# Kernel optimization log

Hardware: AMD Instinct MI355X
Metric: run time of the kernel (lower is better)

## Reference

```python
import jax, jax.numpy as jnp
import numpy as np
import math

IN_F = 1024
OUT_F = 1024
B = 16
L = 4096  # img_size (number of positions)


def setup_inputs() -> dict:
    key = jax.random.key(0)
    k1, k2, k3 = jax.random.split(key, 3)
    Efou = jax.random.normal(k1, (B, L, IN_F), dtype=jnp.float32)
    y = jax.random.normal(k2, (B, IN_F), dtype=jnp.float32)
    weight = jax.random.normal(k3, (1, OUT_F, IN_F, 1), dtype=jnp.float32)
    return {"Efou": Efou, "y": y, "weight": weight}


def reference(Efou, y, weight):
    b, img_size, in_f = Efou.shape
    out_f = weight.shape[1]
    scale = 1.0 / math.sqrt(in_f)
    # per-sample modulated weights: [B, out, in]
    w = scale * weight[:, :, :, 0] * y[:, None, :]
    # demodulation norm over the input-feature axis
    dnorm = jax.lax.rsqrt(jnp.sum(w * w, axis=2, keepdims=True) + 1e-8)  # [B, out, 1]
    w = w * dnorm
    # faithful to torch: Efou.reshape(1, B*in, L) is a raw row-major reshape
    E = Efou.reshape(b, in_f, img_size)  # [B, in, L] (same bytes as original)
    x = jnp.einsum('boi,bil->bol', w, E)  # grouped conv1d, kernel size 1
    # faithful to torch: x.view(B, L, out) is a raw reshape of [B, out, L]
    return x.reshape(b, img_size, out_f)
```

## Files before the change

kernel.cpp:

```cpp
#include <hip/hip_runtime.h>
#include <hip/hip_bf16.h>
#include <cstdint>
#include <cstddef>

typedef __bf16 bf16x8 __attribute__((ext_vector_type(8)));
typedef __bf16 bf16x4 __attribute__((ext_vector_type(4)));
typedef float f32x4 __attribute__((ext_vector_type(4)));

#define BATCH 16
#define MDIM 1024
#define NDIM 4096
#define KDIM 1024
#define BM 256
#define BN 256
#define BK 64
#define NKT (KDIM / BK)

__device__ __forceinline__ void gload_lds16(const void* g, void* l) {
  __builtin_amdgcn_global_load_lds(
      (const __attribute__((address_space(1))) void*)g,
      (__attribute__((address_space(3))) void*)l, 16, 0, 0);
}

#define BAR() __builtin_amdgcn_s_barrier()
#define SB() __builtin_amdgcn_sched_barrier(0)
#define FENCE() asm volatile("" ::: "memory")
#define LGKM0()                                        \
  do {                                                 \
    asm volatile("s_waitcnt lgkmcnt(0)" ::: "memory"); \
    SB();                                              \
  } while (0)
#define VMC32()                                        \
  do {                                                 \
    asm volatile("s_waitcnt vmcnt(32)" ::: "memory");  \
    SB();                                              \
  } while (0)
#define VMC0()                                         \
  do {                                                 \
    asm volatile("s_waitcnt vmcnt(0)" ::: "memory");   \
    SB();                                              \
  } while (0)

__global__ __launch_bounds__(256) void modw_kernel(
    const float* __restrict__ weight, const float* __restrict__ y,
    __bf16* __restrict__ wm) {
  const int blk = blockIdx.x;
  const int b = blk & 15;
  const int o = blk >> 4;
  const int t = threadIdx.x;
  const float4 w4 = reinterpret_cast<const float4*>(weight + (size_t)o * KDIM)[t];
  const float4 y4 = reinterpret_cast<const float4*>(y + (size_t)b * KDIM)[t];
  const float p0 = w4.x * y4.x, p1 = w4.y * y4.y;
  const float p2 = w4.z * y4.z, p3 = w4.w * y4.w;
  float s = p0 * p0 + p1 * p1 + p2 * p2 + p3 * p3;
#pragma unroll
  for (int off = 32; off >= 1; off >>= 1) s += __shfl_xor(s, off, 64);
  __shared__ float ps[4];
  if ((t & 63) == 0) ps[t >> 6] = s;
  __syncthreads();
  const float tot = ps[0] + ps[1] + ps[2] + ps[3];
  const float scale = 0.03125f;
  const float dn = scale * rsqrtf(scale * scale * tot + 1e-8f);
  bf16x4 v;
  v[0] = (__bf16)(p0 * dn);
  v[1] = (__bf16)(p1 * dn);
  v[2] = (__bf16)(p2 * dn);
  v[3] = (__bf16)(p3 * dn);
  *reinterpret_cast<bf16x4*>(wm + ((size_t)b * MDIM + o) * KDIM + t * 4) = v;
}

__global__ __launch_bounds__(512, 2) void gemm_kernel(
    const __bf16* __restrict__ Wm, const float* __restrict__ E,
    float* __restrict__ out) {
  const int orig = blockIdx.x;
  const int wg = (orig & 7) * 128 + (orig >> 3);
  const int mt = wg & 3;
  const int nt = (wg >> 2) & 15;
  const int b = wg >> 6;
  const int m0 = mt * BM, n0 = nt * BN;

  __shared__ __align__(16) char smem[131072];
  char* const A0_ = smem;
  char* const A1_ = smem + 32768;
  char* const B0_ = smem + 65536;
  char* const B1_ = smem + 98304;

  const int tid = threadIdx.x;
  const int lane = tid & 63;
  const int wid = tid >> 6;
  const int wr = wid >> 2;
  const int wc = wid & 3;
  const int ml = lane & 15;
  const int kg = lane >> 4;

  const int arow = tid >> 3;
  const int aswz = ((tid & 7) ^ (arow & 7)) * 8;
  const __bf16* Ag = Wm + ((size_t)(b * MDIM + m0 + arow)) * KDIM + aswz;
  const int aldsOff = tid * 16;

  const int bn1 = tid & 63;
  const int bkg = tid >> 6;
  typedef const __attribute__((address_space(1))) float gfloat;
  gfloat* Eg = (gfloat*)(E + (size_t)b * KDIM * NDIM +
                         (size_t)(bkg * 8) * NDIM + n0 + bn1);
  int bwr[4];
#pragma unroll
  for (int c = 0; c < 4; ++c) {
    const int n = bn1 + 64 * c;
    bwr[c] = n * 128 + ((bkg * 16) ^ ((n & 7) << 4));
  }

  const int colA = (kg * 16) ^ ((ml & 7) << 4);
  const int arB = (wr * 128 + ml) * 128;
  const int brB = (wc * 64 + ml) * 128;

  f32x4 acc[8][4];
#pragma unroll
  for (int i = 0; i < 8; ++i)
#pragma unroll
    for (int j = 0; j < 4; ++j) acc[i][j] = (f32x4){0.f, 0.f, 0.f, 0.f};

  auto stageA = [&](char* Ab, int kt) {
#pragma unroll
    for (int r = 0; r < 4; ++r)
      gload_lds16(Ag + (size_t)(64 * r) * KDIM + kt * BK,
                  Ab + aldsOff + r * 8192);
  };
  auto loadB = [&](float (&brr)[4][8], int kt) {
#pragma unroll
    for (int c = 0; c < 4; ++c)
#pragma unroll
      for (int j = 0; j < 8; ++j)
        brr[c][j] = Eg[(size_t)(kt * BK + j) * NDIM + 64 * c];
  };
  auto writeB = [&](char* Bb, float (&brr)[4][8]) {
#pragma unroll
    for (int c = 0; c < 4; ++c) {
      bf16x8 v;
#pragma unroll
      for (int j = 0; j < 8; ++j) v[j] = (__bf16)brr[c][j];
      *reinterpret_cast<bf16x8*>(Bb + bwr[c]) = v;
    }
  };
  auto rdA = [&](bf16x8 (&d)[4], const char* Ab, int qm, int kk) {
#pragma unroll
    for (int i = 0; i < 4; ++i)
      d[i] = *reinterpret_cast<const bf16x8*>(Ab + arB + (qm * 4 + i) * 2048 +
                                              (colA ^ (kk * 64)));
  };
  auto rdB = [&](bf16x8 (&d)[4], const char* Bb, int kk) {
#pragma unroll
    for (int nf = 0; nf < 4; ++nf)
      d[nf] = *reinterpret_cast<const bf16x8*>(Bb + brB + nf * 2048 +
                                               (colA ^ (kk * 64)));
  };
  auto mfma16 = [&](bf16x8 (&a)[4], bf16x8 (&bv)[4], int qm) {
    __builtin_amdgcn_s_setprio(1);
#pragma unroll
    for (int i = 0; i < 4; ++i)
#pragma unroll
      for (int nf = 0; nf < 4; ++nf)
        acc[qm * 4 + i][nf] = __builtin_amdgcn_mfma_f32_16x16x32_bf16(
            a[i], bv[nf], acc[qm * 4 + i][nf], 0, 0, 0);
    __builtin_amdgcn_s_setprio(0);
  };

  float br[4][8];
  bf16x8 af0[4], af1[4];
  bf16x8 bf0[4], bf1[4];

  {
    float brT[4][8];
    stageA(A0_, 0);
    FENCE();
    loadB(brT, 0);
    writeB(B0_, brT);
    loadB(br, 1);
    LGKM0();
    BAR();
    rdA(af0, A0_, 0, 0);
    rdB(bf0, B0_, 0);
  }

  char* Ac = A0_;
  char* Ao = A1_;
  char* Bc = B0_;
  char* Bo = B1_;

#pragma unroll 1
  for (int t = 0; t < NKT; ++t) {
    const bool pf1 = (t + 1 < NKT);
    const bool pf2 = (t + 2 < NKT);

    rdA(af1, Ac, 1, 0);
    if (pf1) writeB(Bo, br);
    mfma16(af0, bf0, 0);

    rdB(bf1, Bc, 1);
    rdA(af0, Ac, 0, 1);
    if (pf1) stageA(Ao, t + 1);
    FENCE();
    if (pf2) loadB(br, t + 2);
    mfma16(af1, bf0, 1);

    rdA(af1, Ac, 1, 1);
    mfma16(af0, bf1, 0);
    LGKM0();
    if (pf2) {
      VMC32();
    } else {
      VMC0();
    }
    BAR();

    if (pf1) {
      rdA(af0, Ao, 0, 0);
      rdB(bf0, Bo, 0);
    }
    mfma16(af1, bf1, 1);

    char* ta = Ac; Ac = Ao; Ao = ta;
    char* tb = Bc; Bc = Bo; Bo = tb;
  }

  float* ob = out + ((size_t)(b * MDIM + m0 + wr * 128 + kg * 4)) * NDIM +
              n0 + wc * 64 + ml;
#pragma unroll
  for (int mf = 0; mf < 8; ++mf)
#pragma unroll
    for (int nf = 0; nf < 4; ++nf) {
      const f32x4 a = acc[mf][nf];
      float* p = ob + (size_t)mf * 16 * NDIM + nf * 16;
#pragma unroll
      for (int q = 0; q < 4; ++q) p[(size_t)q * NDIM] = a[q];
    }
}

extern "C" void kernel_launch(void* const* d_in, const int* in_sizes, int n_in,
                              void* d_out, int out_size, void* d_ws,
                              size_t ws_size, hipStream_t stream) {
  (void)in_sizes;
  (void)n_in;
  (void)out_size;
  (void)ws_size;
  const float* Efou = (const float*)d_in[0];
  const float* y = (const float*)d_in[1];
  const float* weight = (const float*)d_in[2];
  float* outp = (float*)d_out;
  __bf16* wm = (__bf16*)d_ws;

  modw_kernel<<<dim3(BATCH * MDIM), dim3(256), 0, stream>>>(weight, y, wm);
  gemm_kernel<<<dim3(BATCH * (MDIM / BM) * (NDIM / BN)), dim3(512), 0,
                stream>>>(wm, Efou, outp);
}
```

Measured before the change: 211.6 us.

## Triple-buffer the A tile in LDS with prefetch distance two, drop tail branches

Adds a third LDS buffer for the bf16 weight tile so A is staged two K-steps ahead, matching the register prefetch depth of the fp32 E loads. The tail-iteration branches are removed by wrapping the prefetch index, so every iteration issues the same 36 global loads and can use a fixed vmcnt(36) wait. This is meant to give A loads more time in flight and to keep the loop body uniform. In exchange, the last two iterations fetch data that is never used, and LDS use grows to 160KB per block.

```diff
diff --git a/kernel.cpp b/kernel.cpp
--- a/kernel.cpp
+++ b/kernel.cpp
@@ -30,14 +30,9 @@
     asm volatile("s_waitcnt lgkmcnt(0)" ::: "memory"); \
     SB();                                              \
   } while (0)
-#define VMC32()                                        \
+#define VMC36()                                        \
   do {                                                 \
-    asm volatile("s_waitcnt vmcnt(32)" ::: "memory");  \
-    SB();                                              \
-  } while (0)
-#define VMC0()                                         \
-  do {                                                 \
-    asm volatile("s_waitcnt vmcnt(0)" ::: "memory");   \
+    asm volatile("s_waitcnt vmcnt(36)" ::: "memory");  \
     SB();                                              \
   } while (0)
 
@@ -79,11 +74,12 @@
   const int b = wg >> 6;
   const int m0 = mt * BM, n0 = nt * BN;
 
-  __shared__ __align__(16) char smem[131072];
+  __shared__ __align__(16) char smem[163840];
   char* const A0_ = smem;
   char* const A1_ = smem + 32768;
-  char* const B0_ = smem + 65536;
-  char* const B1_ = smem + 98304;
+  char* const A2_ = smem + 65536;
+  char* const B0_ = smem + 98304;
+  char* const B1_ = smem + 131072;
 
   const int tid = threadIdx.x;
   const int lane = tid & 63;
@@ -176,50 +172,46 @@
     loadB(brT, 0);
     writeB(B0_, brT);
     loadB(br, 1);
+    FENCE();
+    stageA(A1_, 1);
     LGKM0();
     BAR();
     rdA(af0, A0_, 0, 0);
     rdB(bf0, B0_, 0);
   }
 
-  char* Ac = A0_;
-  char* Ao = A1_;
+  char* Acur = A0_;
+  char* Anxt = A1_;
+  char* Astg = A2_;
   char* Bc = B0_;
   char* Bo = B1_;
 
 #pragma unroll 1
   for (int t = 0; t < NKT; ++t) {
-    const bool pf1 = (t + 1 < NKT);
-    const bool pf2 = (t + 2 < NKT);
-
-    rdA(af1, Ac, 1, 0);
-    if (pf1) writeB(Bo, br);
+    const int t2 = (t + 2 < NKT) ? t + 2 : (t + 2 - NKT);
+
+    rdA(af1, Acur, 1, 0);
+    writeB(Bo, br);
     mfma16(af0, bf0, 0);
 
+    loadB(br, t2);
+    FENCE();
     rdB(bf1, Bc, 1);
-    rdA(af0, Ac, 0, 1);
-    if (pf1) stageA(Ao, t + 1);
-    FENCE();
-    if (pf2) loadB(br, t + 2);
+    rdA(af0, Acur, 0, 1);
+    stageA(Astg, t2);
     mfma16(af1, bf0, 1);
 
-    rdA(af1, Ac, 1, 1);
+    rdA(af1, Acur, 1, 1);
     mfma16(af0, bf1, 0);
     LGKM0();
-    if (pf2) {
-      VMC32();
-    } else {
-      VMC0();
-    }
+    VMC36();
     BAR();
 
-    if (pf1) {
-      rdA(af0, Ao, 0, 0);
-      rdB(bf0, Bo, 0);
-    }
+    rdA(af0, Anxt, 0, 0);
+    rdB(bf0, Bo, 0);
     mfma16(af1, bf1, 1);
 
-    char* ta = Ac; Ac = Ao; Ao = ta;
+    char* ta = Acur; Acur = Anxt; Anxt = Astg; Astg = ta;
     char* tb = Bc; Bc = Bo; Bo = tb;
   }
 
```

Result: no change. 212.5 us (+0.4%).

## Load A operand fragments directly from global memory instead of staging through LDS

Applied to the files above, without the earlier changes.

Removes the LDS double-buffer for the modulated-weight A tile and has each wave load its MFMA A fragments straight from global memory into registers. LDS use is halved and the explicit vmcnt waits and async global-to-LDS copies are dropped. In exchange, A data is no longer shared across the four column waves, so each block makes redundant global/L2 reads of A. Global-load latency now sits directly in the MFMA dependency chain, with only compiler-inserted waits to cover it.

```diff
diff --git a/kernel.cpp b/kernel.cpp
--- a/kernel.cpp
+++ b/kernel.cpp
@@ -16,28 +16,11 @@
 #define BK 64
 #define NKT (KDIM / BK)
 
-__device__ __forceinline__ void gload_lds16(const void* g, void* l) {
-  __builtin_amdgcn_global_load_lds(
-      (const __attribute__((address_space(1))) void*)g,
-      (__attribute__((address_space(3))) void*)l, 16, 0, 0);
-}
-
 #define BAR() __builtin_amdgcn_s_barrier()
 #define SB() __builtin_amdgcn_sched_barrier(0)
-#define FENCE() asm volatile("" ::: "memory")
 #define LGKM0()                                        \
   do {                                                 \
     asm volatile("s_waitcnt lgkmcnt(0)" ::: "memory"); \
-    SB();                                              \
-  } while (0)
-#define VMC32()                                        \
-  do {                                                 \
-    asm volatile("s_waitcnt vmcnt(32)" ::: "memory");  \
-    SB();                                              \
-  } while (0)
-#define VMC0()                                         \
-  do {                                                 \
-    asm volatile("s_waitcnt vmcnt(0)" ::: "memory");   \
     SB();                                              \
   } while (0)
 
@@ -79,11 +62,9 @@
   const int b = wg >> 6;
   const int m0 = mt * BM, n0 = nt * BN;
 
-  __shared__ __align__(16) char smem[131072];
-  char* const A0_ = smem;
-  char* const A1_ = smem + 32768;
-  char* const B0_ = smem + 65536;
-  char* const B1_ = smem + 98304;
+  __shared__ __align__(16) char smem[65536];
+  char* const B0_ = smem;
+  char* const B1_ = smem + 32768;
 
   const int tid = threadIdx.x;
   const int lane = tid & 63;
@@ -93,10 +74,8 @@
   const int ml = lane & 15;
   const int kg = lane >> 4;
 
-  const int arow = tid >> 3;
-  const int aswz = ((tid & 7) ^ (arow & 7)) * 8;
-  const __bf16* Ag = Wm + ((size_t)(b * MDIM + m0 + arow)) * KDIM + aswz;
-  const int aldsOff = tid * 16;
+  const __bf16* AgW =
+      Wm + ((size_t)(b * MDIM + m0 + wr * 128 + ml)) * KDIM + kg * 8;
 
   const int bn1 = tid & 63;
   const int bkg = tid >> 6;
@@ -111,7 +90,6 @@
   }
 
   const int colA = (kg * 16) ^ ((ml & 7) << 4);
-  const int arB = (wr * 128 + ml) * 128;
   const int brB = (wc * 64 + ml) * 128;
 
   f32x4 acc[8][4];
@@ -120,12 +98,6 @@
 #pragma unroll
     for (int j = 0; j < 4; ++j) acc[i][j] = (f32x4){0.f, 0.f, 0.f, 0.f};
 
-  auto stageA = [&](char* Ab, int kt) {
-#pragma unroll
-    for (int r = 0; r < 4; ++r)
-      gload_lds16(Ag + (size_t)(64 * r) * KDIM + kt * BK,
-                  Ab + aldsOff + r * 8192);
-  };
   auto loadB = [&](float (&brr)[4][8], int kt) {
 #pragma unroll
     for (int c = 0; c < 4; ++c)
@@ -142,11 +114,11 @@
       *reinterpret_cast<bf16x8*>(Bb + bwr[c]) = v;
     }
   };
-  auto rdA = [&](bf16x8 (&d)[4], const char* Ab, int qm, int kk) {
+  auto gldA = [&](bf16x8 (&d)[4], int kt, int qm, int kk) {
+    const __bf16* base = AgW + (size_t)(qm * 64) * KDIM + kt * 64 + kk * 32;
 #pragma unroll
     for (int i = 0; i < 4; ++i)
-      d[i] = *reinterpret_cast<const bf16x8*>(Ab + arB + (qm * 4 + i) * 2048 +
-                                              (colA ^ (kk * 64)));
+      d[i] = *reinterpret_cast<const bf16x8*>(base + (size_t)(i * 16) * KDIM);
   };
   auto rdB = [&](bf16x8 (&d)[4], const char* Bb, int kk) {
 #pragma unroll
@@ -171,19 +143,15 @@
 
   {
     float brT[4][8];
-    stageA(A0_, 0);
-    FENCE();
     loadB(brT, 0);
     writeB(B0_, brT);
     loadB(br, 1);
     LGKM0();
     BAR();
-    rdA(af0, A0_, 0, 0);
+    gldA(af0, 0, 0, 0);
     rdB(bf0, B0_, 0);
   }
 
-  char* Ac = A0_;
-  char* Ao = A1_;
   char* Bc = B0_;
   char* Bo = B1_;
 
@@ -192,34 +160,26 @@
     const bool pf1 = (t + 1 < NKT);
     const bool pf2 = (t + 2 < NKT);
 
-    rdA(af1, Ac, 1, 0);
+    gldA(af1, t, 1, 0);
     if (pf1) writeB(Bo, br);
     mfma16(af0, bf0, 0);
 
     rdB(bf1, Bc, 1);
-    rdA(af0, Ac, 0, 1);
-    if (pf1) stageA(Ao, t + 1);
-    FENCE();
+    gldA(af0, t, 0, 1);
     if (pf2) loadB(br, t + 2);
     mfma16(af1, bf0, 1);
 
-    rdA(af1, Ac, 1, 1);
+    gldA(af1, t, 1, 1);
     mfma16(af0, bf1, 0);
     LGKM0();
-    if (pf2) {
-      VMC32();
-    } else {
-      VMC0();
-    }
     BAR();
 
     if (pf1) {
-      rdA(af0, Ao, 0, 0);
+      gldA(af0, t + 1, 0, 0);
       rdB(bf0, Bo, 0);
     }
     mfma16(af1, bf1, 1);
 
-    char* ta = Ac; Ac = Ao; Ao = ta;
     char* tb = Bc; Bc = Bo; Bo = tb;
   }
 
```

Result: slower. 368.3 us (+74.0%).
